# Kernel tuning notes

Hardware: AMD Instinct MI355X
Metric: run time of the kernel (lower is better)

Reference implementation:

```python
import jax, jax.numpy as jnp
import numpy as np

ALPHA = 32.0
RANK = 16


def setup_inputs() -> dict:
    key = jax.random.key(0)
    ks = jax.random.split(key, 6)
    d_in, d_out, r = 4096, 4096, RANK
    x = jax.random.normal(ks[0], (4, 2048, d_in), dtype=jnp.float32)
    W = jax.random.normal(ks[1], (d_out, d_in), dtype=jnp.float32) * (1.0 / np.sqrt(d_in))
    bias = jax.random.normal(ks[2], (d_out,), dtype=jnp.float32) * 0.02
    B_lora = jax.random.normal(ks[3], (d_out, r), dtype=jnp.float32) * (1.0 / np.sqrt(r))
    A_lora = jax.random.normal(ks[4], (r, d_in), dtype=jnp.float32) * (1.0 / np.sqrt(d_in))
    delta_bias = jax.random.normal(ks[5], (d_out,), dtype=jnp.float32) * 0.02
    return {"x": x, "W": W, "bias": bias, "B_lora": B_lora, "A_lora": A_lora, "delta_bias": delta_bias}


def reference(x, W, bias, B_lora, A_lora, delta_bias):
    # LoRALinear.forward with adapter_enabled=True:
    # y = x @ (W + (alpha/rank) * B @ A).T + bias + (alpha/rank) * delta_bias
    # Expressed as base GEMM + two small low-rank GEMMs (same math, no
    # [out, in] delta-weight materialization).
    scale = ALPHA / RANK
    base = jnp.einsum('bsi,oi->bso', x, W)              # [B,S,out]
    xa = jnp.einsum('bsi,ri->bsr', x, A_lora)           # [B,S,r]
    delta = jnp.einsum('bsr,or->bso', xa, B_lora)       # [B,S,out]
    return base + scale * delta + bias + scale * delta_bias
```

## Files before the change

kernel.cpp:

```cpp
#include <hip/hip_runtime.h>
#include <stdint.h>

#define M_DIM 8192
#define N_DIM 4096
#define K_DIM 4096

typedef __attribute__((ext_vector_type(4))) float f32x4;
typedef __attribute__((ext_vector_type(8))) __bf16 bf16x8;

__device__ __forceinline__ unsigned short f2bf(float f) {
  unsigned int u = __builtin_bit_cast(unsigned int, f);
  u += 0x7FFFu + ((u >> 16) & 1u);
  return (unsigned short)(u >> 16);
}

__device__ __forceinline__ void load16_lds(const void* g, void* l) {
  __builtin_amdgcn_global_load_lds(
      (__attribute__((address_space(1))) void*)g,
      (__attribute__((address_space(3))) void*)l,
      16, 0, 0);
}

__global__ __launch_bounds__(256) void cvt_x_kernel(const float* __restrict__ x,
                                                    unsigned short* __restrict__ xb) {
  const int n8 = (M_DIM * K_DIM) / 8;
  int i = blockIdx.x * blockDim.x + threadIdx.x;
  const int stride = gridDim.x * blockDim.x;
  for (; i < n8; i += stride) {
    const float4* p = (const float4*)x + (size_t)i * 2;
    const float4 a = p[0];
    const float4 b = p[1];
    uint4 o;
    o.x = (unsigned)f2bf(a.x) | ((unsigned)f2bf(a.y) << 16);
    o.y = (unsigned)f2bf(a.z) | ((unsigned)f2bf(a.w) << 16);
    o.z = (unsigned)f2bf(b.x) | ((unsigned)f2bf(b.y) << 16);
    o.w = (unsigned)f2bf(b.z) | ((unsigned)f2bf(b.w) << 16);
    ((uint4*)xb)[i] = o;
  }
}

__global__ __launch_bounds__(256) void build_wb_kernel(const float* __restrict__ W,
                                                       const float* __restrict__ B_lora,
                                                       const float* __restrict__ A_lora,
                                                       unsigned short* __restrict__ wb) {
  __shared__ float As[64][17];
  __shared__ float Bs[64][17];
  const int t = threadIdx.x;
  const int i0 = blockIdx.x * 64;
  const int o0 = blockIdx.y * 64;
  {
    const int c = t & 63;
    #pragma unroll
    for (int rr = (t >> 6); rr < 16; rr += 4)
      As[c][rr] = A_lora[rr * K_DIM + i0 + c];
    const int r2 = t & 15;
    #pragma unroll
    for (int oo = (t >> 4); oo < 64; oo += 16)
      Bs[oo][r2] = B_lora[(o0 + oo) * 16 + r2];
  }
  __syncthreads();
  const int ci = t & 63;
  const int og = t >> 6;
  float areg[16];
  #pragma unroll
  for (int r = 0; r < 16; ++r) areg[r] = As[ci][r];
  const int i = i0 + ci;
  #pragma unroll 4
  for (int j = 0; j < 16; ++j) {
    const int ol = og * 16 + j;
    float d = 0.f;
    #pragma unroll
    for (int r = 0; r < 16; ++r) d += Bs[ol][r] * areg[r];
    const size_t idx = (size_t)(o0 + ol) * K_DIM + i;
    wb[idx] = f2bf(W[idx] + 2.0f * d);
  }
}

__global__ __launch_bounds__(256) void gemm_kernel(const unsigned short* __restrict__ xb,
                                                   const unsigned short* __restrict__ wb,
                                                   const float* __restrict__ bias,
                                                   const float* __restrict__ dbias,
                                                   float* __restrict__ out) {
  constexpr int BM = 128, BN = 128, BK = 32;
  __shared__ unsigned short As[BM * BK];
  __shared__ unsigned short Bs[BN * BK];

  const int t = threadIdx.x;
  const int w = t >> 6, l = t & 63;
  const int nbn = N_DIM / BN;
  const int nwg = (M_DIM / BM) * nbn;
  int bid = (int)blockIdx.x;
  bid = (bid & 7) * (nwg >> 3) + (bid >> 3);
  const int m0 = (bid / nbn) * BM;
  const int n0 = (bid % nbn) * BN;
  const int wr = w >> 1, wc = w & 1;

  f32x4 acc[4][4];
  #pragma unroll
  for (int i = 0; i < 4; ++i)
    #pragma unroll
    for (int j = 0; j < 4; ++j) acc[i][j] = f32x4{0.f, 0.f, 0.f, 0.f};

  const int q0 = w * 64 + l, q1 = q0 + 256;
  const unsigned short* ga0 = xb + (size_t)(m0 + (q0 >> 2)) * K_DIM + (q0 & 3) * 8;
  const unsigned short* ga1 = xb + (size_t)(m0 + (q1 >> 2)) * K_DIM + (q1 & 3) * 8;
  const unsigned short* gb0 = wb + (size_t)(n0 + (q0 >> 2)) * K_DIM + (q0 & 3) * 8;
  const unsigned short* gb1 = wb + (size_t)(n0 + (q1 >> 2)) * K_DIM + (q1 & 3) * 8;
  unsigned short* la0 = As + w * 512;
  unsigned short* la1 = As + (4 + w) * 512;
  unsigned short* lb0 = Bs + w * 512;
  unsigned short* lb1 = Bs + (4 + w) * 512;

  const unsigned short* pa = As + ((wr * 64 + (l & 15)) * BK + (l >> 4) * 8);
  const unsigned short* pb = Bs + ((wc * 64 + (l & 15)) * BK + (l >> 4) * 8);

  for (int kt = 0; kt < K_DIM; kt += BK) {
    load16_lds(ga0 + kt, la0);
    load16_lds(ga1 + kt, la1);
    load16_lds(gb0 + kt, lb0);
    load16_lds(gb1 + kt, lb1);
    __syncthreads();
    bf16x8 af[4], bfv[4];
    #pragma unroll
    for (int mf = 0; mf < 4; ++mf) af[mf] = *(const bf16x8*)(pa + mf * 16 * BK);
    #pragma unroll
    for (int nf = 0; nf < 4; ++nf) bfv[nf] = *(const bf16x8*)(pb + nf * 16 * BK);
    #pragma unroll
    for (int mf = 0; mf < 4; ++mf)
      #pragma unroll
      for (int nf = 0; nf < 4; ++nf)
        acc[mf][nf] = __builtin_amdgcn_mfma_f32_16x16x32_bf16(af[mf], bfv[nf], acc[mf][nf], 0, 0, 0);
    __syncthreads();
  }

  float bv[4];
  #pragma unroll
  for (int nf = 0; nf < 4; ++nf) {
    const int c = n0 + wc * 64 + nf * 16 + (l & 15);
    bv[nf] = bias[c] + 2.0f * dbias[c];
  }
  #pragma unroll
  for (int mf = 0; mf < 4; ++mf) {
    const int r0 = m0 + wr * 64 + mf * 16 + ((l >> 4) << 2);
    #pragma unroll
    for (int nf = 0; nf < 4; ++nf) {
      const int c = n0 + wc * 64 + nf * 16 + (l & 15);
      const f32x4 v = acc[mf][nf];
      #pragma unroll
      for (int j = 0; j < 4; ++j)
        out[(size_t)(r0 + j) * N_DIM + c] = v[j] + bv[nf];
    }
  }
}

__global__ __launch_bounds__(256) void xa_kernel(const float* __restrict__ x,
                                                 const float* __restrict__ A_lora,
                                                 float* __restrict__ xa) {
  const int m = blockIdx.x;
  const int t = threadIdx.x;
  float acc[16];
  #pragma unroll
  for (int r = 0; r < 16; ++r) acc[r] = 0.f;
  const float* xr = x + (size_t)m * K_DIM;
  for (int k = t; k < K_DIM; k += 256) {
    const float xv = xr[k];
    #pragma unroll
    for (int r = 0; r < 16; ++r) acc[r] += xv * A_lora[r * K_DIM + k];
  }
  __shared__ float red[16][4];
  #pragma unroll
  for (int r = 0; r < 16; ++r) {
    float v = acc[r];
    for (int off = 32; off > 0; off >>= 1) v += __shfl_down(v, off, 64);
    if ((t & 63) == 0) red[r][t >> 6] = v;
  }
  __syncthreads();
  if (t < 16) xa[(size_t)m * 16 + t] = red[t][0] + red[t][1] + red[t][2] + red[t][3];
}

__global__ __launch_bounds__(256) void fgemm_kernel(const float* __restrict__ x,
                                                    const float* __restrict__ W,
                                                    const float* __restrict__ bias,
                                                    const float* __restrict__ B_lora,
                                                    const float* __restrict__ dbias,
                                                    const float* __restrict__ xa,
                                                    float* __restrict__ out) {
  __shared__ float As[64][17];
  __shared__ float Ws[64][17];
  const int t = threadIdx.x;
  const int m0 = (blockIdx.x >> 6) * 64;
  const int n0 = (blockIdx.x & 63) * 64;
  const int tx = t & 15, ty = t >> 4;
  float c[4][4] = {};
  for (int kt = 0; kt < K_DIM; kt += 16) {
    #pragma unroll
    for (int e = 0; e < 4; ++e) {
      const int q = t + e * 256;
      const int r = q >> 4, k = q & 15;
      As[r][k] = x[(size_t)(m0 + r) * K_DIM + kt + k];
      Ws[r][k] = W[(size_t)(n0 + r) * K_DIM + kt + k];
    }
    __syncthreads();
    #pragma unroll
    for (int k = 0; k < 16; ++k) {
      float a[4], b[4];
      #pragma unroll
      for (int ii = 0; ii < 4; ++ii) a[ii] = As[ty * 4 + ii][k];
      #pragma unroll
      for (int jj = 0; jj < 4; ++jj) b[jj] = Ws[tx * 4 + jj][k];
      #pragma unroll
      for (int ii = 0; ii < 4; ++ii)
        #pragma unroll
        for (int jj = 0; jj < 4; ++jj) c[ii][jj] += a[ii] * b[jj];
    }
    __syncthreads();
  }
  #pragma unroll
  for (int ii = 0; ii < 4; ++ii) {
    const int row = m0 + ty * 4 + ii;
    #pragma unroll
    for (int jj = 0; jj < 4; ++jj) {
      const int col = n0 + tx * 4 + jj;
      float d = 0.f;
      #pragma unroll
      for (int r = 0; r < 16; ++r) d += xa[(size_t)row * 16 + r] * B_lora[col * 16 + r];
      out[(size_t)row * N_DIM + col] = c[ii][jj] + 2.0f * d + bias[col] + 2.0f * dbias[col];
    }
  }
}

extern "C" void kernel_launch(void* const* d_in, const int* in_sizes, int n_in,
                              void* d_out, int out_size, void* d_ws, size_t ws_size,
                              hipStream_t stream) {
  const float* x = (const float*)d_in[0];
  const float* W = (const float*)d_in[1];
  const float* bias = (const float*)d_in[2];
  const float* B_lora = (const float*)d_in[3];
  const float* A_lora = (const float*)d_in[4];
  const float* dbias = (const float*)d_in[5];
  float* out = (float*)d_out;

  const size_t NEED = (size_t)M_DIM * K_DIM * 2 + (size_t)N_DIM * K_DIM * 2;
  if (ws_size >= NEED) {
    unsigned short* xb = (unsigned short*)d_ws;
    unsigned short* wb = xb + (size_t)M_DIM * K_DIM;
    cvt_x_kernel<<<2048, 256, 0, stream>>>(x, xb);
    build_wb_kernel<<<dim3(64, 64), 256, 0, stream>>>(W, B_lora, A_lora, wb);
    gemm_kernel<<<2048, 256, 0, stream>>>(xb, wb, bias, dbias, out);
  } else {
    float* xa = (float*)d_ws;
    xa_kernel<<<M_DIM, 256, 0, stream>>>(x, A_lora, xa);
    fgemm_kernel<<<(M_DIM / 64) * (N_DIM / 64), 256, 0, stream>>>(x, W, bias, B_lora, dbias, xa, out);
  }
}
```

Baseline: 629.1 us.

## Rewrite bf16 GEMM as 256x256 double-buffered, swizzled, interleaved MFMA pipeline

Replaces the 128x128 single-buffer GEMM with a 256x256 tile, BK=64, 512-thread kernel. LDS is double-buffered, and the next tile's global-to-LDS loads are interleaved with four MFMA quadrants using explicit vmcnt waits and barriers. LDS addresses are XOR-swizzled to avoid bank conflicts, and MFMA sections run at raised priority. The goal is to hide memory latency and raise data reuse per load. The cost is 128KB of LDS, which limits occupancy, and hand-tuned waitcnt ordering that is fragile to get right.

Result: faster. 557.9 us (-11.3%).

```diff
diff --git a/kernel.cpp b/kernel.cpp
--- a/kernel.cpp
+++ b/kernel.cpp
@@ -20,6 +20,9 @@
       (__attribute__((address_space(3))) void*)l,
       16, 0, 0);
 }
+
+#define WAITVM(N) asm volatile("s_waitcnt vmcnt(" #N ")" ::: "memory")
+#define BARRIER() asm volatile("s_barrier" ::: "memory")
 
 __global__ __launch_bounds__(256) void cvt_x_kernel(const float* __restrict__ x,
                                                     unsigned short* __restrict__ xb) {
@@ -76,62 +79,119 @@
   }
 }
 
-__global__ __launch_bounds__(256) void gemm_kernel(const unsigned short* __restrict__ xb,
-                                                   const unsigned short* __restrict__ wb,
-                                                   const float* __restrict__ bias,
-                                                   const float* __restrict__ dbias,
-                                                   float* __restrict__ out) {
-  constexpr int BM = 128, BN = 128, BK = 32;
-  __shared__ unsigned short As[BM * BK];
-  __shared__ unsigned short Bs[BN * BK];
+__global__ __launch_bounds__(512, 2) void gemm_kernel(const unsigned short* __restrict__ xb,
+                                                      const unsigned short* __restrict__ wb,
+                                                      const float* __restrict__ bias,
+                                                      const float* __restrict__ dbias,
+                                                      float* __restrict__ out) {
+  constexpr int BK = 64;
+  constexpr int NT = K_DIM / BK;
+  __shared__ char As[65536];
+  __shared__ char Bs[65536];
 
   const int t = threadIdx.x;
   const int w = t >> 6, l = t & 63;
-  const int nbn = N_DIM / BN;
-  const int nwg = (M_DIM / BM) * nbn;
+  const int wr = w >> 2, wc = w & 3;
+  constexpr int NBN = N_DIM / 256;
+  constexpr int NWG = (M_DIM / 256) * NBN;
   int bid = (int)blockIdx.x;
-  bid = (bid & 7) * (nwg >> 3) + (bid >> 3);
-  const int m0 = (bid / nbn) * BM;
-  const int n0 = (bid % nbn) * BN;
-  const int wr = w >> 1, wc = w & 1;
-
-  f32x4 acc[4][4];
-  #pragma unroll
-  for (int i = 0; i < 4; ++i)
+  bid = (bid & 7) * (NWG >> 3) + (bid >> 3);
+  const int m0 = (bid / NBN) * 256;
+  const int n0 = (bid % NBN) * 256;
+
+  const int trow = t >> 3;
+  const int scol = ((t & 7) ^ (trow & 7)) * 8;
+  const int rowoffA[4] = {0, 128, 64, 192};
+  const int ldsoffA[4] = {0, 16384, 8192, 24576};
+  const unsigned short* gAp[4];
+  #pragma unroll
+  for (int j = 0; j < 4; ++j)
+    gAp[j] = xb + (size_t)(m0 + rowoffA[j] + trow) * K_DIM + scol;
+  const unsigned short* gBp[4];
+  #pragma unroll
+  for (int j = 0; j < 4; ++j) {
+    const int rp = j * 64 + trow;
+    const int gr = (rp & 31) + ((rp >> 5) & 3) * 64 + (rp >> 7) * 32;
+    gBp[j] = wb + (size_t)(n0 + gr) * K_DIM + scol;
+  }
+  const int wlds = w * 1024;
+
+  const int swz = (l & 7) << 4;
+  const int rdk = (l >> 4) * 16;
+  const int rdA = (wr * 128 + (l & 15)) * 128;
+  const int rdB = (wc * 32 + (l & 15)) * 128;
+
+  f32x4 acc[8][4];
+  #pragma unroll
+  for (int i = 0; i < 8; ++i)
     #pragma unroll
     for (int j = 0; j < 4; ++j) acc[i][j] = f32x4{0.f, 0.f, 0.f, 0.f};
-
-  const int q0 = w * 64 + l, q1 = q0 + 256;
-  const unsigned short* ga0 = xb + (size_t)(m0 + (q0 >> 2)) * K_DIM + (q0 & 3) * 8;
-  const unsigned short* ga1 = xb + (size_t)(m0 + (q1 >> 2)) * K_DIM + (q1 & 3) * 8;
-  const unsigned short* gb0 = wb + (size_t)(n0 + (q0 >> 2)) * K_DIM + (q0 & 3) * 8;
-  const unsigned short* gb1 = wb + (size_t)(n0 + (q1 >> 2)) * K_DIM + (q1 & 3) * 8;
-  unsigned short* la0 = As + w * 512;
-  unsigned short* la1 = As + (4 + w) * 512;
-  unsigned short* lb0 = Bs + w * 512;
-  unsigned short* lb1 = Bs + (4 + w) * 512;
-
-  const unsigned short* pa = As + ((wr * 64 + (l & 15)) * BK + (l >> 4) * 8);
-  const unsigned short* pb = Bs + ((wc * 64 + (l & 15)) * BK + (l >> 4) * 8);
-
-  for (int kt = 0; kt < K_DIM; kt += BK) {
-    load16_lds(ga0 + kt, la0);
-    load16_lds(ga1 + kt, la1);
-    load16_lds(gb0 + kt, lb0);
-    load16_lds(gb1 + kt, lb1);
-    __syncthreads();
-    bf16x8 af[4], bfv[4];
-    #pragma unroll
-    for (int mf = 0; mf < 4; ++mf) af[mf] = *(const bf16x8*)(pa + mf * 16 * BK);
-    #pragma unroll
-    for (int nf = 0; nf < 4; ++nf) bfv[nf] = *(const bf16x8*)(pb + nf * 16 * BK);
-    #pragma unroll
-    for (int mf = 0; mf < 4; ++mf)
-      #pragma unroll
-      for (int nf = 0; nf < 4; ++nf)
-        acc[mf][nf] = __builtin_amdgcn_mfma_f32_16x16x32_bf16(af[mf], bfv[nf], acc[mf][nf], 0, 0, 0);
-    __syncthreads();
-  }
+  bf16x8 af[4][2], bf[4][2];
+
+#define STAGE_A(CUR, SLOT, KT) \
+  load16_lds(gAp[SLOT] + (KT), As + (CUR) * 32768 + ldsoffA[SLOT] + wlds)
+#define STAGE_B(CUR, SLOT, KT) \
+  load16_lds(gBp[SLOT] + (KT), Bs + (CUR) * 32768 + (SLOT) * 8192 + wlds)
+
+#define READ_AH(CUR, MH)                                                      \
+  {                                                                           \
+    const char* base_ = As + (CUR) * 32768 + rdA + (MH) * 8192;               \
+    _Pragma("unroll") for (int mf_ = 0; mf_ < 4; ++mf_)                       \
+      _Pragma("unroll") for (int ks_ = 0; ks_ < 2; ++ks_)                     \
+        af[mf_][ks_] = *(const bf16x8*)(base_ + mf_ * 2048 +                  \
+                                        ((ks_ * 64 + rdk) ^ swz));            \
+  }
+#define READ_BH(CUR, NH)                                                      \
+  {                                                                           \
+    const char* base_ = Bs + (CUR) * 32768 + rdB + (NH) * 16384;              \
+    _Pragma("unroll") for (int nf_ = 0; nf_ < 2; ++nf_)                       \
+      _Pragma("unroll") for (int ks_ = 0; ks_ < 2; ++ks_)                     \
+        bf[(NH) * 2 + nf_][ks_] = *(const bf16x8*)(base_ + nf_ * 2048 +       \
+                                                   ((ks_ * 64 + rdk) ^ swz)); \
+  }
+#define QUAD(MH, NH)                                                          \
+  {                                                                           \
+    __builtin_amdgcn_s_setprio(1);                                            \
+    _Pragma("unroll") for (int mf_ = 0; mf_ < 4; ++mf_)                       \
+      _Pragma("unroll") for (int nf_ = 0; nf_ < 2; ++nf_)                     \
+        _Pragma("unroll") for (int ks_ = 0; ks_ < 2; ++ks_)                   \
+          acc[(MH) * 4 + mf_][(NH) * 2 + nf_] =                               \
+              __builtin_amdgcn_mfma_f32_16x16x32_bf16(                        \
+                  af[mf_][ks_], bf[(NH) * 2 + nf_][ks_],                      \
+                  acc[(MH) * 4 + mf_][(NH) * 2 + nf_], 0, 0, 0);              \
+    __builtin_amdgcn_s_setprio(0);                                            \
+  }
+
+  STAGE_A(0, 0, 0); STAGE_A(0, 1, 0);
+  STAGE_B(0, 0, 0); STAGE_B(0, 1, 0);
+  STAGE_B(0, 2, 0); STAGE_B(0, 3, 0);
+  STAGE_A(0, 2, 0); STAGE_A(0, 3, 0);
+  WAITVM(4);
+  BARRIER();
+
+  int cur = 0;
+  for (int kt = 0; kt < NT - 1; ++kt) {
+    const int kn = (kt + 1) * BK;
+    const int nxt = cur ^ 1;
+    READ_AH(cur, 0); READ_BH(cur, 0);
+    STAGE_A(nxt, 0, kn); STAGE_A(nxt, 1, kn);
+    BARRIER(); QUAD(0, 0); WAITVM(4); BARRIER();
+    READ_BH(cur, 1);
+    STAGE_B(nxt, 0, kn); STAGE_B(nxt, 1, kn);
+    BARRIER(); QUAD(0, 1); WAITVM(4); BARRIER();
+    READ_AH(cur, 1);
+    STAGE_B(nxt, 2, kn); STAGE_B(nxt, 3, kn);
+    BARRIER(); QUAD(1, 1); BARRIER();
+    STAGE_A(nxt, 2, kn); STAGE_A(nxt, 3, kn);
+    BARRIER(); QUAD(1, 0); WAITVM(4); BARRIER();
+    cur = nxt;
+  }
+  READ_AH(cur, 0); READ_BH(cur, 0);
+  BARRIER(); QUAD(0, 0); WAITVM(2); BARRIER();
+  READ_BH(cur, 1);
+  BARRIER(); QUAD(0, 1); WAITVM(0); BARRIER();
+  READ_AH(cur, 1);
+  QUAD(1, 1); QUAD(1, 0);
 
   float bv[4];
   #pragma unroll
@@ -140,8 +200,8 @@
     bv[nf] = bias[c] + 2.0f * dbias[c];
   }
   #pragma unroll
-  for (int mf = 0; mf < 4; ++mf) {
-    const int r0 = m0 + wr * 64 + mf * 16 + ((l >> 4) << 2);
+  for (int mf = 0; mf < 8; ++mf) {
+    const int r0 = m0 + wr * 128 + mf * 16 + ((l >> 4) << 2);
     #pragma unroll
     for (int nf = 0; nf < 4; ++nf) {
       const int c = n0 + wc * 64 + nf * 16 + (l & 15);
@@ -151,6 +211,11 @@
         out[(size_t)(r0 + j) * N_DIM + c] = v[j] + bv[nf];
     }
   }
+#undef STAGE_A
+#undef STAGE_B
+#undef READ_AH
+#undef READ_BH
+#undef QUAD
 }
 
 __global__ __launch_bounds__(256) void xa_kernel(const float* __restrict__ x,
@@ -246,7 +311,7 @@
     unsigned short* wb = xb + (size_t)M_DIM * K_DIM;
     cvt_x_kernel<<<2048, 256, 0, stream>>>(x, xb);
     build_wb_kernel<<<dim3(64, 64), 256, 0, stream>>>(W, B_lora, A_lora, wb);
-    gemm_kernel<<<2048, 256, 0, stream>>>(xb, wb, bias, dbias, out);
+    gemm_kernel<<<(M_DIM / 256) * (N_DIM / 256), 512, 0, stream>>>(xb, wb, bias, dbias, out);
   } else {
     float* xa = (float*)d_ws;
     xa_kernel<<<M_DIM, 256, 0, stream>>>(x, A_lora, xa);
```
